# Kernel tuning notes

Hardware: AMD Instinct MI355X
Metric: run time of the kernel (lower is better)

## Reference

```python
import jax, jax.numpy as jnp
import numpy as np

EPS = 1e-9  # projective normalization epsilon
LN_EPS = 1e-5


def setup_inputs() -> dict:
    N, E, Fin, Fout = 50000, 600000, 128, 128
    key = jax.random.key(0)
    ks = jax.random.split(key, 8)
    x = jax.random.normal(ks[0], (N, Fin), jnp.float32)
    edge_index = jax.random.randint(ks[1], (2, E), 0, N, dtype=jnp.int64)
    edge_weight = jax.random.normal(ks[2], (E,), jnp.float32)
    W_self = jax.random.normal(ks[3], (Fin, Fout), jnp.float32) / np.sqrt(Fin)
    b_self = jnp.zeros((Fout,), jnp.float32)
    W_nb = jax.random.normal(ks[4], (Fin, Fout), jnp.float32) / np.sqrt(Fin)
    b_nb = jnp.zeros((Fout,), jnp.float32)
    gamma = jnp.ones((Fout,), jnp.float32)
    beta = jnp.zeros((Fout,), jnp.float32)
    return dict(x=x, edge_index=edge_index, edge_weight=edge_weight,
                W_self=W_self, b_self=b_self, W_nb=W_nb, b_nb=b_nb,
                gamma=gamma, beta=beta)


def _proj_normalize(v):
    # UHG projective_average tail: L2-normalize the weighted sum
    return v / (jnp.linalg.norm(v, axis=-1, keepdims=True) + EPS)


def reference(x, edge_index, edge_weight, W_self, b_self, W_nb, b_nb, gamma, beta):
    N = x.shape[0]
    src, tgt = edge_index[0], edge_index[1]

    # --- neighbor aggregation: per-target softmax over edge weights, then
    # weighted projective average of gathered source features (vectorized
    # replacement of the per-node python loop) ---
    seg_max = jax.ops.segment_max(edge_weight, tgt, num_segments=N)  # [N]
    ew = jnp.exp(edge_weight - seg_max[tgt])                          # [E]
    denom = jax.ops.segment_sum(ew, tgt, num_segments=N)              # [N]
    alpha = ew / denom[tgt]                                           # softmax per target
    agg = jax.ops.segment_sum(alpha[:, None] * x[src], tgt, num_segments=N)  # [N, Fin]
    agg = _proj_normalize(agg)  # isolated nodes stay exactly zero (0 / eps)

    # --- self / neighbor linear transforms ---
    self_feat = x @ W_self + b_self    # [N, Fout]
    nb_feat = agg @ W_nb + b_nb        # [N, Fout]

    # --- combine: projective average with weights [0.5, 0.5] ---
    comb = _proj_normalize(0.5 * (self_feat + nb_feat))

    # --- UHG layer norm (standard layernorm over feature dim) ---
    mu = jnp.mean(comb, axis=-1, keepdims=True)
    var = jnp.var(comb, axis=-1, keepdims=True)
    out = (comb - mu) / jnp.sqrt(var + LN_EPS) * gamma + beta
    # dropout is identity in eval mode
    return out
```

## Files before the change

### kernel.cpp

```cpp
#include <hip/hip_runtime.h>
#include <hip/hip_bf16.h>
#include <hip/hip_fp16.h>

#define EPS 1e-9f
#define LN_EPS 1e-5f

typedef __attribute__((ext_vector_type(8))) short bf16x8;
typedef __attribute__((ext_vector_type(4))) float f32x4;

__device__ __forceinline__ float lo16(unsigned p) { return __uint_as_float(p << 16); }
__device__ __forceinline__ float hi16(unsigned p) { return __uint_as_float(p & 0xffff0000u); }
__device__ __forceinline__ unsigned f2b(float f) {
    unsigned u = __float_as_uint(f);
    return (u + 0x7fffu + ((u >> 16) & 1u)) >> 16;
}
__device__ __forceinline__ int eidx(const int* ei, size_t i, int i64) {
    return i64 ? ei[2 * i] : ei[i];
}
__device__ __forceinline__ float ldw(const float* fp, const __hip_bfloat16* hp, int i, int f32) {
    return f32 ? fp[i] : __bfloat162float(hp[i]);
}

__global__ void prep(const unsigned* __restrict__ xb, const float4* __restrict__ xf4,
                     uint2* __restrict__ xcvt2, const int* __restrict__ ei,
                     const unsigned* __restrict__ Wsb, const float* __restrict__ Wsf,
                     const unsigned* __restrict__ Wnb, const float* __restrict__ Wnf,
                     unsigned* __restrict__ wt, int4* __restrict__ count4,
                     int* __restrict__ flags, int* __restrict__ ticket,
                     int n4, int zb, int N4z) {
    __shared__ int sf[2];
    if (threadIdx.x < 64) {
        int lane = threadIdx.x;
        unsigned d = xb[lane * 97];
        unsigned ex = (d >> 7) & 0xFFu;
        unsigned long long m1 = __ballot(ex >= 110u && ex <= 135u);
        int hi = ei[2 * lane + 1];
        unsigned long long m2 = __ballot(hi == 0);
        if (lane == 0) {
            sf[0] = (__popcll(m1) > 32) ? 0 : 1;
            sf[1] = (__popcll(m2) > 32) ? 1 : 0;
        }
    }
    __syncthreads();
    int f32 = sf[0];
    int b = blockIdx.x;
    if (b == 0 && threadIdx.x == 0) { flags[0] = sf[0]; flags[1] = sf[1]; }
    if (b < 64) {
        int tid = b * 256 + threadIdx.x;
        int f = tid >> 7, k2 = tid & 127;
        int k2l = k2 & 63;
        unsigned out;
        if (f32) {
            const float* W = (k2 < 64) ? Wsf : Wnf;
            float lo = W[(2 * k2l) * 128 + f], hi = W[(2 * k2l + 1) * 128 + f];
            out = f2b(lo) | (f2b(hi) << 16);
        } else {
            const unsigned* W = (k2 < 64) ? Wsb : Wnb;
            unsigned lo = W[(2 * k2l) * 64 + (f >> 1)];
            unsigned hi = W[(2 * k2l + 1) * 64 + (f >> 1)];
            unsigned a = (f & 1) ? (lo >> 16) : (lo & 0xffffu);
            unsigned b2 = (f & 1) ? (hi & 0xffff0000u) : (hi << 16);
            out = a | b2;
        }
        wt[tid] = out;
    } else if (b < 64 + zb) {
        int i = (b - 64) * 256 + threadIdx.x;
        if (i < N4z) count4[i] = make_int4(0, 0, 0, 0);
        if (b == 64 && threadIdx.x == 0) *ticket = 0;
    } else {
        if (!f32) return;
        int i = (b - 64 - zb) * 256 + threadIdx.x;
        if (i >= n4) return;
        float4 v = xf4[i];
        xcvt2[i] = make_uint2(f2b(v.x) | (f2b(v.y) << 16), f2b(v.z) | (f2b(v.w) << 16));
    }
}

__global__ void edge_count(const int* __restrict__ ei, int* __restrict__ count,
                           int* __restrict__ tgt32, int* __restrict__ rank,
                           const int* __restrict__ flags, int E) {
    int e0 = (blockIdx.x * 256 + threadIdx.x) * 4;
    if (e0 >= E) return;
    int i64 = flags[1];
    if (e0 + 4 <= E) {
        int t0, t1, t2, t3;
        if (i64 && !(E & 1)) {
            const int4* q = (const int4*)(ei + 2 * (size_t)(E + e0));
            int4 a = q[0], b = q[1];
            t0 = a.x; t1 = a.z; t2 = b.x; t3 = b.z;
        } else if (!i64 && !(E & 3)) {
            int4 a = *(const int4*)(ei + (size_t)E + e0);
            t0 = a.x; t1 = a.y; t2 = a.z; t3 = a.w;
        } else {
            t0 = eidx(ei, (size_t)E + e0 + 0, i64); t1 = eidx(ei, (size_t)E + e0 + 1, i64);
            t2 = eidx(ei, (size_t)E + e0 + 2, i64); t3 = eidx(ei, (size_t)E + e0 + 3, i64);
        }
        int r0 = atomicAdd(&count[t0], 1), r1 = atomicAdd(&count[t1], 1),
            r2 = atomicAdd(&count[t2], 1), r3 = atomicAdd(&count[t3], 1);
        *(int4*)(tgt32 + e0) = make_int4(t0, t1, t2, t3);
        *(int4*)(rank + e0)  = make_int4(r0, r1, r2, r3);
    } else {
        for (int j = 0; j < 4 && e0 + j < E; ++j) {
            int t = eidx(ei, (size_t)E + e0 + j, i64);
            rank[e0 + j] = atomicAdd(&count[t], 1);
            tgt32[e0 + j] = t;
        }
    }
}

__global__ void scan_blocks(const int* __restrict__ count, int* __restrict__ offsets,
                            int* __restrict__ bsum, int* __restrict__ bpre,
                            int* __restrict__ ticket, int N, int B) {
    __shared__ int wsum[16];
    int tid = threadIdx.x, lane = tid & 63, w = tid >> 6;
    int i0 = blockIdx.x * 4096 + tid * 4;
    int4 v;
    if (i0 + 3 < N) v = *(const int4*)(count + i0);
    else {
        v.x = (i0     < N) ? count[i0]     : 0;
        v.y = (i0 + 1 < N) ? count[i0 + 1] : 0;
        v.z = (i0 + 2 < N) ? count[i0 + 2] : 0;
        v.w = (i0 + 3 < N) ? count[i0 + 3] : 0;
    }
    int s = v.x + v.y + v.z + v.w;
    int incl = s;
    #pragma unroll
    for (int off = 1; off < 64; off <<= 1) {
        int t = __shfl_up(incl, off);
        if (lane >= off) incl += t;
    }
    if (lane == 63) wsum[w] = incl;
    __syncthreads();
    int wpre = 0, tot = 0;
    #pragma unroll
    for (int j = 0; j < 16; ++j) { int sj = wsum[j]; if (j < w) wpre += sj; tot += sj; }
    int o0 = wpre + incl - s;
    int o1 = o0 + v.x, o2 = o1 + v.y, o3 = o2 + v.z;
    if (i0 + 3 < N) {
        *(int4*)(offsets + i0) = make_int4(o0, o1, o2, o3);
    } else {
        if (i0     < N) offsets[i0]     = o0;
        if (i0 + 1 < N) offsets[i0 + 1] = o1;
        if (i0 + 2 < N) offsets[i0 + 2] = o2;
    }
    if (tid == 0) {
        bsum[blockIdx.x] = tot;
        __threadfence();
        int t = atomicAdd(ticket, 1);
        if (t == B - 1) {
            int run = 0;
            for (int j = 0; j < B; ++j) {
                int vj = atomicAdd(&bsum[j], 0);
                bpre[j] = run; run += vj;
            }
            bpre[B] = run;
            offsets[N] = (N & 4095) ? (run - bpre[B - 1]) : 0;
        }
    }
}

template <int PACK>
__global__ void edge_scatter(const int* __restrict__ ei, const int* __restrict__ tgt32,
                             const int* __restrict__ rank,
                             const float* __restrict__ ewf, const __hip_bfloat16* __restrict__ ewh,
                             const int* __restrict__ offsets, const int* __restrict__ bpre,
                             unsigned* __restrict__ csr4, uint2* __restrict__ csr8,
                             const int* __restrict__ flags, int E) {
    int e0 = (blockIdx.x * 256 + threadIdx.x) * 4;
    if (e0 >= E) return;
    int f32 = flags[0], i64 = flags[1];
    if (e0 + 4 <= E) {
        int4 t = *(const int4*)(tgt32 + e0);
        int4 r = *(const int4*)(rank + e0);
        int s0, s1, s2, s3;
        if (i64) {
            const int4* q = (const int4*)(ei + 2 * (size_t)e0);
            int4 a = q[0], b = q[1];
            s0 = a.x; s1 = a.z; s2 = b.x; s3 = b.z;
        } else if (!(e0 & 3)) {
            int4 a = *(const int4*)(ei + e0);
            s0 = a.x; s1 = a.y; s2 = a.z; s3 = a.w;
        } else {
            s0 = ei[e0]; s1 = ei[e0 + 1]; s2 = ei[e0 + 2]; s3 = ei[e0 + 3];
        }
        float w0 = ldw(ewf, ewh, e0 + 0, f32), w1 = ldw(ewf, ewh, e0 + 1, f32),
              w2 = ldw(ewf, ewh, e0 + 2, f32), w3 = ldw(ewf, ewh, e0 + 3, f32);
        int o0 = offsets[t.x] + bpre[t.x >> 12] + r.x,
            o1 = offsets[t.y] + bpre[t.y >> 12] + r.y,
            o2 = offsets[t.z] + bpre[t.z >> 12] + r.z,
            o3 = offsets[t.w] + bpre[t.w >> 12] + r.w;
        float a0 = expf(w0), a1 = expf(w1), a2 = expf(w2), a3 = expf(w3);
        if (PACK) {
            csr4[o0] = (unsigned)s0 | ((unsigned)__half_as_ushort(__float2half(a0)) << 16);
            csr4[o1] = (unsigned)s1 | ((unsigned)__half_as_ushort(__float2half(a1)) << 16);
            csr4[o2] = (unsigned)s2 | ((unsigned)__half_as_ushort(__float2half(a2)) << 16);
            csr4[o3] = (unsigned)s3 | ((unsigned)__half_as_ushort(__float2half(a3)) << 16);
        } else {
            csr8[o0] = make_uint2((unsigned)s0, __float_as_uint(a0));
            csr8[o1] = make_uint2((unsigned)s1, __float_as_uint(a1));
            csr8[o2] = make_uint2((unsigned)s2, __float_as_uint(a2));
            csr8[o3] = make_uint2((unsigned)s3, __float_as_uint(a3));
        }
    } else {
        for (int j = 0; j < 4 && e0 + j < E; ++j) {
            int e = e0 + j;
            int t = tgt32[e];
            int s = eidx(ei, e, i64);
            float al = expf(ldw(ewf, ewh, e, f32));
            int pos = offsets[t] + bpre[t >> 12] + rank[e];
            if (PACK) csr4[pos] = (unsigned)s | ((unsigned)__half_as_ushort(__float2half(al)) << 16);
            else      csr8[pos] = make_uint2((unsigned)s, __float_as_uint(al));
        }
    }
}

template <int PACK>
__device__ __forceinline__ void dec_edge(const unsigned* __restrict__ c4,
                                         const uint2* __restrict__ c8, int j,
                                         unsigned& s, float& al) {
    if (PACK) {
        unsigned r = c4[j];
        s = r & 0xffffu;
        al = __half2float(__ushort_as_half((unsigned short)(r >> 16)));
    } else {
        uint2 e = c8[j];
        s = e.x;
        al = __uint_as_float(e.y);
    }
}

template <int PACK>
__global__ void aggregate(const unsigned* __restrict__ xb, const unsigned* __restrict__ xcvt,
                          const int* __restrict__ offsets, const int* __restrict__ bpre,
                          const unsigned* __restrict__ csr4, const uint2* __restrict__ csr8,
                          unsigned* __restrict__ aggb, const int* __restrict__ flags, int N) {
    int node = blockIdx.x * 4 + (threadIdx.x >> 6);
    if (node >= N) return;
    int lane = threadIdx.x & 63;
    const unsigned* xs = flags[0] ? xcvt : xb;
    float a0 = 0.f, a1 = 0.f;
    int beg = offsets[node] + bpre[node >> 12];
    int end = offsets[node + 1] + bpre[(node + 1) >> 12];
    for (int j = beg; j < end; j += 8) {
        int last = end - 1;
        int j0 = j,     i0 = (j0 < end) ? j0 : last;
        int j1 = j + 1, i1 = (j1 < end) ? j1 : last;
        int j2 = j + 2, i2 = (j2 < end) ? j2 : last;
        int j3 = j + 3, i3 = (j3 < end) ? j3 : last;
        int j4 = j + 4, i4 = (j4 < end) ? j4 : last;
        int j5 = j + 5, i5 = (j5 < end) ? j5 : last;
        int j6 = j + 6, i6 = (j6 < end) ? j6 : last;
        int j7 = j + 7, i7 = (j7 < end) ? j7 : last;
        unsigned s0, s1, s2, s3, s4, s5, s6, s7;
        float l0, l1, l2, l3, l4, l5, l6, l7;
        dec_edge<PACK>(csr4, csr8, i0, s0, l0); dec_edge<PACK>(csr4, csr8, i1, s1, l1);
        dec_edge<PACK>(csr4, csr8, i2, s2, l2); dec_edge<PACK>(csr4, csr8, i3, s3, l3);
        dec_edge<PACK>(csr4, csr8, i4, s4, l4); dec_edge<PACK>(csr4, csr8, i5, s5, l5);
        dec_edge<PACK>(csr4, csr8, i6, s6, l6); dec_edge<PACK>(csr4, csr8, i7, s7, l7);
        unsigned p0 = xs[s0 * 64 + lane], p1 = xs[s1 * 64 + lane],
                 p2 = xs[s2 * 64 + lane], p3 = xs[s3 * 64 + lane],
                 p4 = xs[s4 * 64 + lane], p5 = xs[s5 * 64 + lane],
                 p6 = xs[s6 * 64 + lane], p7 = xs[s7 * 64 + lane];
        l1 = (j1 < end) ? l1 : 0.f; l2 = (j2 < end) ? l2 : 0.f;
        l3 = (j3 < end) ? l3 : 0.f; l4 = (j4 < end) ? l4 : 0.f;
        l5 = (j5 < end) ? l5 : 0.f; l6 = (j6 < end) ? l6 : 0.f;
        l7 = (j7 < end) ? l7 : 0.f;
        a0 += l0 * lo16(p0); a1 += l0 * hi16(p0);
        a0 += l1 * lo16(p1); a1 += l1 * hi16(p1);
        a0 += l2 * lo16(p2); a1 += l2 * hi16(p2);
        a0 += l3 * lo16(p3); a1 += l3 * hi16(p3);
        a0 += l4 * lo16(p4); a1 += l4 * hi16(p4);
        a0 += l5 * lo16(p5); a1 += l5 * hi16(p5);
        a0 += l6 * lo16(p6); a1 += l6 * hi16(p6);
        a0 += l7 * lo16(p7); a1 += l7 * hi16(p7);
    }
    float ss = a0 * a0 + a1 * a1;
    #pragma unroll
    for (int m = 32; m >= 1; m >>= 1) ss += __shfl_xor(ss, m);
    float inv = 1.f / (sqrtf(ss) + EPS);
    aggb[node * 64 + lane] = f2b(a0 * inv) | (f2b(a1 * inv) << 16);
}

__global__ __launch_bounds__(128) void fused_mfma(
    const unsigned* __restrict__ xb, const unsigned* __restrict__ xcvt,
    const unsigned* __restrict__ aggb, const uint4* __restrict__ wt4,
    const float* __restrict__ bsf, const __hip_bfloat16* __restrict__ bsh,
    const float* __restrict__ bnf, const __hip_bfloat16* __restrict__ bnh,
    const float* __restrict__ gf, const __hip_bfloat16* __restrict__ gh,
    const float* __restrict__ tf, const __hip_bfloat16* __restrict__ th,
    float* __restrict__ outf, unsigned* __restrict__ outb,
    const int* __restrict__ flags, int N)
{
    __shared__ uint4 sA[1024];
    int f32 = flags[0];
    const uint4* xs4 = (const uint4*)(f32 ? xcvt : xb);
    const uint4* ag4 = (const uint4*)aggb;
    int tid = threadIdx.x;
    int node0 = blockIdx.x * 32;

    #pragma unroll
    for (int i = 0; i < 8; ++i) {
        int ci = i * 128 + tid;
        int r = ci >> 5, c = ci & 31;
        int node = node0 + r;
        uint4 v = make_uint4(0, 0, 0, 0);
        if (node < N) v = (c < 16) ? xs4[node * 16 + c] : ag4[node * 16 + (c - 16)];
        sA[r * 32 + (c ^ (r & 15))] = v;
    }
    __syncthreads();

    int lane = tid & 63, w = tid >> 6, g = lane >> 4, c16 = lane & 15;
    int rloc = w * 16 + c16;

    f32x4 acc[8];
    #pragma unroll
    for (int t = 0; t < 8; ++t) acc[t] = (f32x4){0.f, 0.f, 0.f, 0.f};

    #pragma unroll
    for (int kk = 0; kk < 8; ++kk) {
        uint4 av = sA[rloc * 32 + ((kk * 4 + g) ^ c16)];
        bf16x8 a = __builtin_bit_cast(bf16x8, av);
        #pragma unroll
        for (int t = 0; t < 8; ++t) {
            uint4 bv = wt4[(t * 16 + c16) * 32 + kk * 4 + g];
            bf16x8 b = __builtin_bit_cast(bf16x8, bv);
            acc[t] = __builtin_amdgcn_mfma_f32_16x16x32_bf16(a, b, acc[t], 0, 0, 0);
        }
    }

    float bsum[8], gam[8], bet[8];
    #pragma unroll
    for (int t = 0; t < 8; ++t) {
        int f = t * 16 + c16;
        bsum[t] = ldw(bsf, bsh, f, f32) + ldw(bnf, bnh, f, f32);
        gam[t]  = ldw(gf, gh, f, f32);
        bet[t]  = ldw(tf, th, f, f32);
    }

    #pragma unroll
    for (int reg = 0; reg < 4; ++reg) {
        int node = node0 + w * 16 + g * 4 + reg;
        float cv[8], s1 = 0.f, s2 = 0.f;
        #pragma unroll
        for (int t = 0; t < 8; ++t) {
            float c_ = 0.5f * (acc[t][reg] + bsum[t]);
            cv[t] = c_; s1 += c_; s2 += c_ * c_;
        }
        #pragma unroll
        for (int m = 1; m < 16; m <<= 1) { s1 += __shfl_xor(s1, m); s2 += __shfl_xor(s2, m); }
        float inv  = 1.f / (sqrtf(s2) + EPS);
        float mean = s1 * inv * (1.f / 128.f);
        float var  = s2 * inv * inv * (1.f / 128.f) - mean * mean;
        float rstd = 1.f / sqrtf(var + LN_EPS);
        if (f32) {
            if (node < N) {
                #pragma unroll
                for (int t = 0; t < 8; ++t) {
                    float o = (cv[t] * inv - mean) * rstd * gam[t] + bet[t];
                    outf[(size_t)node * 128 + t * 16 + c16] = o;
                }
            }
        } else {
            #pragma unroll
            for (int t = 0; t < 8; ++t) {
                float o = (cv[t] * inv - mean) * rstd * gam[t] + bet[t];
                float po = __shfl_xor(o, 1);
                if (!(c16 & 1) && node < N)
                    outb[node * 64 + t * 8 + (c16 >> 1)] = f2b(o) | (f2b(po) << 16);
            }
        }
    }
}

static inline size_t rup16(size_t x) { return (x + 15) & ~(size_t)15; }

extern "C" void kernel_launch(void* const* d_in, const int* in_sizes, int n_in,
                              void* d_out, int out_size, void* d_ws, size_t ws_size,
                              hipStream_t stream) {
    int N = in_sizes[0] / 128;
    int E = in_sizes[1] / 2;
    const int* ei = (const int*)d_in[1];

    char* p = (char*)d_ws;
    int* flags = (int*)p;              p += 16;
    int* ticket = (int*)p;             p += 16;
    int* count = (int*)p;              p += rup16((size_t)N * 4);
    int* offsets = (int*)p;            p += rup16((size_t)(N + 4) * 4);
    int* bsum = (int*)p;               p += 256;
    int* bpre = (int*)p;               p += 512;
    int* tgt32 = (int*)p;              p += rup16((size_t)E * 4);
    int* rank = (int*)p;               p += rup16((size_t)E * 4);
    unsigned* csr4 = (unsigned*)p;
    uint2* csr8 = (uint2*)p;           p += rup16((size_t)E * 8);
    unsigned* wt = (unsigned*)p;       p += 128 * 128 * 4;
    unsigned* xcvt = (unsigned*)p;     p += rup16((size_t)N * 64 * 4);
    unsigned* aggb = (unsigned*)p;

    int eb4 = (E + 1023) / 1024;
    int nb = (N + 3) / 4;
    int nbf = (N + 31) / 32;
    int ncv = (N * 32 + 255) / 256;
    int scanB = (N + 4095) / 4096;
    int N4z = (int)(rup16((size_t)N * 4) / 16);
    int zb = (N4z + 255) / 256;
    int pack = (N <= 65536);

    prep<<<64 + zb + ncv, 256, 0, stream>>>((const unsigned*)d_in[0], (const float4*)d_in[0],
                                            (uint2*)xcvt, ei,
                                            (const unsigned*)d_in[3], (const float*)d_in[3],
                                            (const unsigned*)d_in[5], (const float*)d_in[5],
                                            wt, (int4*)count, flags, ticket, N * 32, zb, N4z);
    edge_count<<<eb4, 256, 0, stream>>>(ei, count, tgt32, rank, flags, E);
    scan_blocks<<<scanB, 1024, 0, stream>>>(count, offsets, bsum, bpre, ticket, N, scanB);
    if (pack)
        edge_scatter<1><<<eb4, 256, 0, stream>>>(ei, tgt32, rank, (const float*)d_in[2],
                                                 (const __hip_bfloat16*)d_in[2],
                                                 offsets, bpre, csr4, csr8, flags, E);
    else
        edge_scatter<0><<<eb4, 256, 0, stream>>>(ei, tgt32, rank, (const float*)d_in[2],
                                                 (const __hip_bfloat16*)d_in[2],
                                                 offsets, bpre, csr4, csr8, flags, E);
    if (pack)
        aggregate<1><<<nb, 256, 0, stream>>>((const unsigned*)d_in[0], xcvt,
                                             offsets, bpre, csr4, csr8, aggb, flags, N);
    else
        aggregate<0><<<nb, 256, 0, stream>>>((const unsigned*)d_in[0], xcvt,
                                             offsets, bpre, csr4, csr8, aggb, flags, N);
    fused_mfma<<<nbf, 128, 0, stream>>>((const unsigned*)d_in[0], xcvt, aggb, (const uint4*)wt,
                                        (const float*)d_in[4], (const __hip_bfloat16*)d_in[4],
                                        (const float*)d_in[6], (const __hip_bfloat16*)d_in[6],
                                        (const float*)d_in[7], (const __hip_bfloat16*)d_in[7],
                                        (const float*)d_in[8], (const __hip_bfloat16*)d_in[8],
                                        (float*)d_out, (unsigned*)d_out, flags, N);
}
```

Measured before the change: 202.5 us.

## Process two nodes per wavefront in aggregate and drop tgt32 scratch array

The aggregate kernel now gives each node 32 lanes, each accumulating four bf16 features via 8-byte loads, so one wavefront handles two nodes. This halves the launch size and the per-node shuffle reduction, and allows wider gather loads. Separately, edge_count no longer writes a tgt32 array; edge_scatter re-reads the targets from edge_index instead. That trades an extra read of the index array for removing one E-sized write and read.

```diff
diff --git a/kernel.cpp b/kernel.cpp
--- a/kernel.cpp
+++ b/kernel.cpp
@@ -77,8 +77,7 @@
 }
 
 __global__ void edge_count(const int* __restrict__ ei, int* __restrict__ count,
-                           int* __restrict__ tgt32, int* __restrict__ rank,
-                           const int* __restrict__ flags, int E) {
+                           int* __restrict__ rank, const int* __restrict__ flags, int E) {
     int e0 = (blockIdx.x * 256 + threadIdx.x) * 4;
     if (e0 >= E) return;
     int i64 = flags[1];
@@ -97,13 +96,11 @@
         }
         int r0 = atomicAdd(&count[t0], 1), r1 = atomicAdd(&count[t1], 1),
             r2 = atomicAdd(&count[t2], 1), r3 = atomicAdd(&count[t3], 1);
-        *(int4*)(tgt32 + e0) = make_int4(t0, t1, t2, t3);
-        *(int4*)(rank + e0)  = make_int4(r0, r1, r2, r3);
+        *(int4*)(rank + e0) = make_int4(r0, r1, r2, r3);
     } else {
         for (int j = 0; j < 4 && e0 + j < E; ++j) {
             int t = eidx(ei, (size_t)E + e0 + j, i64);
             rank[e0 + j] = atomicAdd(&count[t], 1);
-            tgt32[e0 + j] = t;
         }
     }
 }
@@ -160,8 +157,7 @@
 }
 
 template <int PACK>
-__global__ void edge_scatter(const int* __restrict__ ei, const int* __restrict__ tgt32,
-                             const int* __restrict__ rank,
+__global__ void edge_scatter(const int* __restrict__ ei, const int* __restrict__ rank,
                              const float* __restrict__ ewf, const __hip_bfloat16* __restrict__ ewh,
                              const int* __restrict__ offsets, const int* __restrict__ bpre,
                              unsigned* __restrict__ csr4, uint2* __restrict__ csr8,
@@ -170,9 +166,8 @@
     if (e0 >= E) return;
     int f32 = flags[0], i64 = flags[1];
     if (e0 + 4 <= E) {
-        int4 t = *(const int4*)(tgt32 + e0);
         int4 r = *(const int4*)(rank + e0);
-        int s0, s1, s2, s3;
+        int t0, t1, t2, t3, s0, s1, s2, s3;
         if (i64) {
             const int4* q = (const int4*)(ei + 2 * (size_t)e0);
             int4 a = q[0], b = q[1];
@@ -183,12 +178,23 @@
         } else {
             s0 = ei[e0]; s1 = ei[e0 + 1]; s2 = ei[e0 + 2]; s3 = ei[e0 + 3];
         }
+        if (i64 && !(E & 1)) {
+            const int4* q = (const int4*)(ei + 2 * (size_t)(E + e0));
+            int4 a = q[0], b = q[1];
+            t0 = a.x; t1 = a.z; t2 = b.x; t3 = b.z;
+        } else if (!i64 && !(E & 3)) {
+            int4 a = *(const int4*)(ei + (size_t)E + e0);
+            t0 = a.x; t1 = a.y; t2 = a.z; t3 = a.w;
+        } else {
+            t0 = eidx(ei, (size_t)E + e0 + 0, i64); t1 = eidx(ei, (size_t)E + e0 + 1, i64);
+            t2 = eidx(ei, (size_t)E + e0 + 2, i64); t3 = eidx(ei, (size_t)E + e0 + 3, i64);
+        }
         float w0 = ldw(ewf, ewh, e0 + 0, f32), w1 = ldw(ewf, ewh, e0 + 1, f32),
               w2 = ldw(ewf, ewh, e0 + 2, f32), w3 = ldw(ewf, ewh, e0 + 3, f32);
-        int o0 = offsets[t.x] + bpre[t.x >> 12] + r.x,
-            o1 = offsets[t.y] + bpre[t.y >> 12] + r.y,
-            o2 = offsets[t.z] + bpre[t.z >> 12] + r.z,
-            o3 = offsets[t.w] + bpre[t.w >> 12] + r.w;
+        int o0 = offsets[t0] + bpre[t0 >> 12] + r.x,
+            o1 = offsets[t1] + bpre[t1 >> 12] + r.y,
+            o2 = offsets[t2] + bpre[t2 >> 12] + r.z,
+            o3 = offsets[t3] + bpre[t3 >> 12] + r.w;
         float a0 = expf(w0), a1 = expf(w1), a2 = expf(w2), a3 = expf(w3);
         if (PACK) {
             csr4[o0] = (unsigned)s0 | ((unsigned)__half_as_ushort(__float2half(a0)) << 16);
@@ -204,7 +210,7 @@
     } else {
         for (int j = 0; j < 4 && e0 + j < E; ++j) {
             int e = e0 + j;
-            int t = tgt32[e];
+            int t = eidx(ei, (size_t)E + e, i64);
             int s = eidx(ei, e, i64);
             float al = expf(ldw(ewf, ewh, e, f32));
             int pos = offsets[t] + bpre[t >> 12] + rank[e];
@@ -233,12 +239,14 @@
 __global__ void aggregate(const unsigned* __restrict__ xb, const unsigned* __restrict__ xcvt,
                           const int* __restrict__ offsets, const int* __restrict__ bpre,
                           const unsigned* __restrict__ csr4, const uint2* __restrict__ csr8,
-                          unsigned* __restrict__ aggb, const int* __restrict__ flags, int N) {
-    int node = blockIdx.x * 4 + (threadIdx.x >> 6);
+                          uint2* __restrict__ aggb2, const int* __restrict__ flags, int N) {
+    int wid = blockIdx.x * 4 + (threadIdx.x >> 6);
+    int half = (threadIdx.x >> 5) & 1;
+    int node = wid * 2 + half;
     if (node >= N) return;
-    int lane = threadIdx.x & 63;
-    const unsigned* xs = flags[0] ? xcvt : xb;
-    float a0 = 0.f, a1 = 0.f;
+    int lane32 = threadIdx.x & 31;
+    const uint2* xs2 = (const uint2*)(flags[0] ? xcvt : xb);
+    float a0 = 0.f, a1 = 0.f, a2 = 0.f, a3 = 0.f;
     int beg = offsets[node] + bpre[node >> 12];
     int end = offsets[node + 1] + bpre[(node + 1) >> 12];
     for (int j = beg; j < end; j += 8) {
@@ -257,28 +265,29 @@
         dec_edge<PACK>(csr4, csr8, i2, s2, l2); dec_edge<PACK>(csr4, csr8, i3, s3, l3);
         dec_edge<PACK>(csr4, csr8, i4, s4, l4); dec_edge<PACK>(csr4, csr8, i5, s5, l5);
         dec_edge<PACK>(csr4, csr8, i6, s6, l6); dec_edge<PACK>(csr4, csr8, i7, s7, l7);
-        unsigned p0 = xs[s0 * 64 + lane], p1 = xs[s1 * 64 + lane],
-                 p2 = xs[s2 * 64 + lane], p3 = xs[s3 * 64 + lane],
-                 p4 = xs[s4 * 64 + lane], p5 = xs[s5 * 64 + lane],
-                 p6 = xs[s6 * 64 + lane], p7 = xs[s7 * 64 + lane];
+        uint2 p0 = xs2[s0 * 32 + lane32], p1 = xs2[s1 * 32 + lane32],
+              p2 = xs2[s2 * 32 + lane32], p3 = xs2[s3 * 32 + lane32],
+              p4 = xs2[s4 * 32 + lane32], p5 = xs2[s5 * 32 + lane32],
+              p6 = xs2[s6 * 32 + lane32], p7 = xs2[s7 * 32 + lane32];
         l1 = (j1 < end) ? l1 : 0.f; l2 = (j2 < end) ? l2 : 0.f;
         l3 = (j3 < end) ? l3 : 0.f; l4 = (j4 < end) ? l4 : 0.f;
         l5 = (j5 < end) ? l5 : 0.f; l6 = (j6 < end) ? l6 : 0.f;
         l7 = (j7 < end) ? l7 : 0.f;
-        a0 += l0 * lo16(p0); a1 += l0 * hi16(p0);
-        a0 += l1 * lo16(p1); a1 += l1 * hi16(p1);
-        a0 += l2 * lo16(p2); a1 += l2 * hi16(p2);
-        a0 += l3 * lo16(p3); a1 += l3 * hi16(p3);
-        a0 += l4 * lo16(p4); a1 += l4 * hi16(p4);
-        a0 += l5 * lo16(p5); a1 += l5 * hi16(p5);
-        a0 += l6 * lo16(p6); a1 += l6 * hi16(p6);
-        a0 += l7 * lo16(p7); a1 += l7 * hi16(p7);
-    }
-    float ss = a0 * a0 + a1 * a1;
-    #pragma unroll
-    for (int m = 32; m >= 1; m >>= 1) ss += __shfl_xor(ss, m);
+        a0 += l0 * lo16(p0.x); a1 += l0 * hi16(p0.x); a2 += l0 * lo16(p0.y); a3 += l0 * hi16(p0.y);
+        a0 += l1 * lo16(p1.x); a1 += l1 * hi16(p1.x); a2 += l1 * lo16(p1.y); a3 += l1 * hi16(p1.y);
+        a0 += l2 * lo16(p2.x); a1 += l2 * hi16(p2.x); a2 += l2 * lo16(p2.y); a3 += l2 * hi16(p2.y);
+        a0 += l3 * lo16(p3.x); a1 += l3 * hi16(p3.x); a2 += l3 * lo16(p3.y); a3 += l3 * hi16(p3.y);
+        a0 += l4 * lo16(p4.x); a1 += l4 * hi16(p4.x); a2 += l4 * lo16(p4.y); a3 += l4 * hi16(p4.y);
+        a0 += l5 * lo16(p5.x); a1 += l5 * hi16(p5.x); a2 += l5 * lo16(p5.y); a3 += l5 * hi16(p5.y);
+        a0 += l6 * lo16(p6.x); a1 += l6 * hi16(p6.x); a2 += l6 * lo16(p6.y); a3 += l6 * hi16(p6.y);
+        a0 += l7 * lo16(p7.x); a1 += l7 * hi16(p7.x); a2 += l7 * lo16(p7.y); a3 += l7 * hi16(p7.y);
+    }
+    float ss = a0 * a0 + a1 * a1 + a2 * a2 + a3 * a3;
+    #pragma unroll
+    for (int m = 16; m >= 1; m >>= 1) ss += __shfl_xor(ss, m);
     float inv = 1.f / (sqrtf(ss) + EPS);
-    aggb[node * 64 + lane] = f2b(a0 * inv) | (f2b(a1 * inv) << 16);
+    aggb2[node * 32 + lane32] = make_uint2(f2b(a0 * inv) | (f2b(a1 * inv) << 16),
+                                           f2b(a2 * inv) | (f2b(a3 * inv) << 16));
 }
 
 __global__ __launch_bounds__(128) void fused_mfma(
@@ -388,7 +397,6 @@
     int* offsets = (int*)p;            p += rup16((size_t)(N + 4) * 4);
     int* bsum = (int*)p;               p += 256;
     int* bpre = (int*)p;               p += 512;
-    int* tgt32 = (int*)p;              p += rup16((size_t)E * 4);
     int* rank = (int*)p;               p += rup16((size_t)E * 4);
     unsigned* csr4 = (unsigned*)p;
     uint2* csr8 = (uint2*)p;           p += rup16((size_t)E * 8);
@@ -397,7 +405,7 @@
     unsigned* aggb = (unsigned*)p;
 
     int eb4 = (E + 1023) / 1024;
-    int nb = (N + 3) / 4;
+    int nb2 = (N + 7) / 8;
     int nbf = (N + 31) / 32;
     int ncv = (N * 32 + 255) / 256;
     int scanB = (N + 4095) / 4096;
@@ -410,22 +418,22 @@
                                             (const unsigned*)d_in[3], (const float*)d_in[3],
                                             (const unsigned*)d_in[5], (const float*)d_in[5],
                                             wt, (int4*)count, flags, ticket, N * 32, zb, N4z);
-    edge_count<<<eb4, 256, 0, stream>>>(ei, count, tgt32, rank, flags, E);
+    edge_count<<<eb4, 256, 0, stream>>>(ei, count, rank, flags, E);
     scan_blocks<<<scanB, 1024, 0, stream>>>(count, offsets, bsum, bpre, ticket, N, scanB);
     if (pack)
-        edge_scatter<1><<<eb4, 256, 0, stream>>>(ei, tgt32, rank, (const float*)d_in[2],
+        edge_scatter<1><<<eb4, 256, 0, stream>>>(ei, rank, (const float*)d_in[2],
                                                  (const __hip_bfloat16*)d_in[2],
                                                  offsets, bpre, csr4, csr8, flags, E);
     else
-        edge_scatter<0><<<eb4, 256, 0, stream>>>(ei, tgt32, rank, (const float*)d_in[2],
+        edge_scatter<0><<<eb4, 256, 0, stream>>>(ei, rank, (const float*)d_in[2],
                                                  (const __hip_bfloat16*)d_in[2],
                                                  offsets, bpre, csr4, csr8, flags, E);
     if (pack)
-        aggregate<1><<<nb, 256, 0, stream>>>((const unsigned*)d_in[0], xcvt,
-                                             offsets, bpre, csr4, csr8, aggb, flags, N);
+        aggregate<1><<<nb2, 256, 0, stream>>>((const unsigned*)d_in[0], xcvt,
+                                              offsets, bpre, csr4, csr8, (uint2*)aggb, flags, N);
     else
-        aggregate<0><<<nb, 256, 0, stream>>>((const unsigned*)d_in[0], xcvt,
-                                             offsets, bpre, csr4, csr8, aggb, flags, N);
+        aggregate<0><<<nb2, 256, 0, stream>>>((const unsigned*)d_in[0], xcvt,
+                                              offsets, bpre, csr4, csr8, (uint2*)aggb, flags, N);
     fused_mfma<<<nbf, 128, 0, stream>>>((const unsigned*)d_in[0], xcvt, aggb, (const uint4*)wt,
                                         (const float*)d_in[4], (const __hip_bfloat16*)d_in[4],
                                         (const float*)d_in[6], (const __hip_bfloat16*)d_in[6],
```

After: 202.8 us. Within noise of the previous version (+0.2%).
